# Kernel tuning notes

Hardware: AMD Instinct MI355X
Metric: run time of the kernel (lower is better)

## Reference

```python
import jax, jax.numpy as jnp
import numpy as np

EPS = 1e-5  # BatchNorm eps (torch default); BN is in training mode with gamma=1, beta=0 (init values)


def bn(x, axes):
    m = jnp.mean(x, axis=axes, keepdims=True)
    v = jnp.var(x, axis=axes, keepdims=True)
    return (x - m) * jax.lax.rsqrt(v + EPS)


def knn_idx(xyz, k):
    # brute-force squared-distance matrix [B,N,N], k smallest
    d = jnp.sum((xyz[:, :, None, :] - xyz[:, None, :, :]) ** 2, axis=-1)
    _, idx = jax.lax.top_k(-d, k)
    return idx  # [B,N,k]


def gather(x, idx):
    # x: [B,N,C], idx: [B,N,k] -> [B,N,k,C]
    return jax.vmap(lambda a, i: a[i])(x, idx)


def lse(xyz, features, idx, w):
    nbr_xyz = gather(xyz, idx)                       # [B,N,k,3]
    rel = nbr_xyz - xyz[:, :, None, :]
    dist = jnp.sqrt(jnp.maximum(jnp.sum(rel ** 2, -1, keepdims=True), 1e-12))
    nbr_f = gather(features, idx)                    # [B,N,k,C]
    enc = jnp.concatenate([rel, dist, nbr_f], -1)    # [B,N,k,C+4]
    return jax.nn.relu(bn(jnp.einsum('bnkc,oc->bnko', enc, w), (0, 1, 2)))


def att_pool(x, sw1, sw2, sb2, mw):
    # x: [B,N,k,C]
    h = jax.nn.relu(bn(jnp.einsum('bnkc,oc->bnko', x, sw1), (0, 1, 2)))
    scores = jax.nn.softmax(jnp.einsum('bnkc,oc->bnko', h, sw2) + sb2, axis=2)  # softmax over k
    feat = jnp.sum(x * scores, axis=2)               # [B,N,C]
    return jax.nn.relu(bn(jnp.einsum('bnc,oc->bno', feat, mw), (0, 1)))


def drb(x, w1, w2):
    # in_channels == out_channels -> identity shortcut
    h = jax.nn.relu(bn(jnp.einsum('bnc,oc->bno', x, w1), (0, 1)))
    h = bn(jnp.einsum('bnc,oc->bno', h, w2), (0, 1))
    return jax.nn.relu(h + x)


def setup_inputs() -> dict:
    key = jax.random.key(0)
    B, N, C, K, OUT = 4, 8192, 32, 16, 128
    H = OUT // 2  # 64
    ks = jax.random.split(key, 16)
    s = 0.05
    return {
        'xyz': jax.random.normal(ks[0], (B, N, 3), jnp.float32),
        'features': jax.random.normal(ks[1], (B, N, C), jnp.float32),
        'w_lse1': jax.random.normal(ks[2], (H, C + 4), jnp.float32) * s,
        'w_lse2': jax.random.normal(ks[3], (H, C + 4), jnp.float32) * s,
        'ap1_sw1': jax.random.normal(ks[4], (H, H), jnp.float32) * s,
        'ap1_sw2': jax.random.normal(ks[5], (1, H), jnp.float32) * s,
        'ap1_sb2': jax.random.normal(ks[6], (1,), jnp.float32) * s,
        'ap1_mw': jax.random.normal(ks[7], (H, H), jnp.float32) * s,
        'ap2_sw1': jax.random.normal(ks[8], (H, H), jnp.float32) * s,
        'ap2_sw2': jax.random.normal(ks[9], (1, H), jnp.float32) * s,
        'ap2_sb2': jax.random.normal(ks[10], (1,), jnp.float32) * s,
        'ap2_mw': jax.random.normal(ks[11], (H, H), jnp.float32) * s,
        'drb_w1': jax.random.normal(ks[12], (OUT, OUT), jnp.float32) * s,
        'drb_w2': jax.random.normal(ks[13], (OUT, OUT), jnp.float32) * s,
    }


def reference(xyz, features, w_lse1, w_lse2, ap1_sw1, ap1_sw2, ap1_sb2, ap1_mw,
              ap2_sw1, ap2_sw2, ap2_sb2, ap2_mw, drb_w1, drb_w2):
    K = 16
    idx = knn_idx(xyz, K)  # original calls knn twice on same xyz -> identical indices
    f1 = att_pool(lse(xyz, features, idx, w_lse1), ap1_sw1, ap1_sw2, ap1_sb2, ap1_mw)
    f2 = att_pool(lse(xyz, features, idx, w_lse2), ap2_sw1, ap2_sw2, ap2_sb2, ap2_mw)
    agg = jnp.concatenate([f1, f2], axis=-1)  # [B,N,128]
    return drb(agg, drb_w1, drb_w2)           # [B,N,128]
```

## Files before the change

### kernel.cpp

```cpp
#include <hip/hip_runtime.h>
#include <hip/hip_bf16.h>
#include <hip/hip_fp16.h>
#include <float.h>
#include <math.h>

#define DEVFN __device__ __forceinline__

DEVFN void wavefence() { __builtin_amdgcn_wave_barrier(); }

using half8 = __attribute__((ext_vector_type(8))) _Float16;
using f32x4 = __attribute__((ext_vector_type(4))) float;

namespace {
constexpr int Bq = 4, Nq = 8192, Cq = 32, Kq = 16;
constexpr int PTS = Bq * Nq;
constexpr int CH = 16;
constexpr int CAND = Nq / CH;
constexpr double ROWS = 524288.0;

constexpr int DS_Y = 0, DS_Z = 256, DS_G = 512, DS_H1 = 768, DS_H2 = 1024;

constexpr size_t OFF_KD   = 0;
constexpr size_t OFF_KJ   = (size_t)32 << 20;
constexpr size_t OFF_X0   = 0;
constexpr size_t OFF_X1   = (size_t)64 << 20;
constexpr size_t OFF_ENC  = (size_t)128 << 20;
constexpr size_t OFF_H1   = 0;
constexpr size_t OFF_H2   = (size_t)16 << 20;
constexpr size_t OFF_GRAW = (size_t)192 << 20;
constexpr size_t OFF_AGG  = (size_t)208 << 20;
constexpr size_t OFF_IDX  = (size_t)224 << 20;
constexpr size_t OFF_DST  = (size_t)226 << 20;
constexpr size_t OFF_MST  = ((size_t)226 << 20) + 10240;
constexpr size_t OFF_BNP  = ((size_t)226 << 20) + 16384;
constexpr size_t WS_NEED  = ((size_t)226 << 20) + 32768;
constexpr size_t FB_GRAW  = (size_t)64 << 20;
constexpr size_t FB_AGG   = (size_t)80 << 20;
constexpr size_t FB_H1    = (size_t)96 << 20;
constexpr size_t FB_H2    = (size_t)112 << 20;
constexpr size_t FB_IDX   = (size_t)128 << 20;
constexpr size_t FB_DST   = (size_t)130 << 20;
constexpr size_t FB_MST   = ((size_t)130 << 20) + 10240;
constexpr size_t FB_BNP   = ((size_t)130 << 20) + 16384;
}

DEVFN void ce_asc(float& a, float& b) {
  const float lo = fminf(a, b), hi = fmaxf(a, b);
  a = lo; b = hi;
}

DEVFN void topk16_update(float* __restrict__ L, float* __restrict__ d) {
#pragma unroll
  for (int k = 2; k <= 16; k <<= 1) {
#pragma unroll
    for (int j = k >> 1; j > 0; j >>= 1) {
#pragma unroll
      for (int i = 0; i < 16; ++i) {
        const int l = i ^ j;
        if (l > i) {
          if ((i & k) == 0) {
            const float lo = fminf(d[i], d[l]), hi = fmaxf(d[i], d[l]);
            d[i] = lo; d[l] = hi;
          } else {
            const float lo = fminf(d[i], d[l]), hi = fmaxf(d[i], d[l]);
            d[i] = hi; d[l] = lo;
          }
        }
      }
    }
  }
#pragma unroll
  for (int i = 0; i < 16; ++i) L[i] = fminf(L[i], d[15 - i]);
#pragma unroll
  for (int j = 8; j > 0; j >>= 1) {
#pragma unroll
    for (int i = 0; i < 16; ++i) {
      const int l = i ^ j;
      if (l > i) ce_asc(L[i], L[l]);
    }
  }
}

DEVFN float distf(const float4 c, const float qx, const float qy, const float qz) {
  const float dx = qx - c.x, dy = qy - c.y, dz = qz - c.z;
  return __fadd_rn(__fadd_rn(__fmul_rn(dx, dx), __fmul_rn(dy, dy)), __fmul_rn(dz, dz));
}

__global__ __launch_bounds__(256, 4) void knn_chunk_kernel(const float* __restrict__ xyz,
                                                           float* __restrict__ pd,
                                                           int* __restrict__ pj) {
  const int b = blockIdx.z;
  const int ch = blockIdx.y;
  const int n = blockIdx.x * 256 + threadIdx.x;
  __shared__ __align__(16) float4 tile[CAND];
  const float* xb = xyz + (size_t)b * Nq * 3;
  for (int t = threadIdx.x; t < CAND; t += 256) {
    const int j = ch * CAND + t;
    tile[t] = make_float4(xb[j * 3], xb[j * 3 + 1], xb[j * 3 + 2], 0.f);
  }
  __syncthreads();
  const float qx = xb[n * 3], qy = xb[n * 3 + 1], qz = xb[n * 3 + 2];
  float L[16];
#pragma unroll
  for (int i = 0; i < 16; ++i) L[i] = FLT_MAX;
  for (int t = 0; t < CAND; t += 16) {
    float d[16];
#pragma unroll
    for (int u = 0; u < 16; ++u) d[u] = distf(tile[t + u], qx, qy, qz);
    topk16_update(L, d);
  }
  const float kth = L[15];
  const size_t base = (((size_t)b * Nq + n) * CH + ch) * Kq;
  int cnt = 0, tfirst = -1;
  for (int t = 0; t < CAND; ++t) {
    const float d = distf(tile[t], qx, qy, qz);
    if (d < kth) { pd[base + cnt] = d; pj[base + cnt] = ch * CAND + t; ++cnt; }
    tfirst = (d == kth && tfirst < 0) ? t : tfirst;
  }
  if (cnt == 15) {
    pd[base + 15] = kth; pj[base + 15] = ch * CAND + tfirst; cnt = 16;
  }
  if (__any(cnt < 16)) {
    for (int t = 0; t < CAND; ++t) {
      const float d = distf(tile[t], qx, qy, qz);
      if (d == kth && cnt < 16) { pd[base + cnt] = d; pj[base + cnt] = ch * CAND + t; ++cnt; }
    }
  }
}

__global__ __launch_bounds__(256, 4) void knn_merge_kernel(const float* __restrict__ pd,
                                                           const int* __restrict__ pj,
                                                           int* __restrict__ idxo) {
  const int q = blockIdx.x * 256 + threadIdx.x;
  const float* dp = pd + (size_t)q * CH * Kq;
  const int* jp = pj + (size_t)q * CH * Kq;
  float L[16];
#pragma unroll
  for (int i = 0; i < 16; ++i) L[i] = FLT_MAX;
  for (int t = 0; t < CH * Kq; t += 16) {
    float d[16];
#pragma unroll
    for (int u = 0; u < 16; u += 4) {
      const float4 v = *(const float4*)(dp + t + u);
      d[u] = v.x; d[u + 1] = v.y; d[u + 2] = v.z; d[u + 3] = v.w;
    }
    topk16_update(L, d);
  }
  const float kth = L[15];
  int* op = idxo + (size_t)q * Kq;
  int cnt = 0;
  for (int t = 0; t < CH * Kq; ++t) {
    const float d = dp[t];
    if (d < kth) { op[cnt] = jp[t]; ++cnt; }
  }
  for (int t = 0; t < CH * Kq; ++t) {
    const float d = dp[t];
    if (d == kth && cnt < 16) { op[cnt] = jp[t]; ++cnt; }
  }
}

struct PF { float4 f0, f1; float nx, ny, nz; };

DEVFN PF issue_feat(const float* __restrict__ features, const float* __restrict__ xyz,
                    int p, int j, int sub) {
  const int b = p >> 13;
  const float* fr = features + ((size_t)b * Nq + j) * Cq;
  const float* xb = xyz + ((size_t)b * Nq + j) * 3;
  PF r;
  r.f0 = *(const float4*)(fr + sub * 8);
  r.f1 = *(const float4*)(fr + sub * 8 + 4);
  r.nx = xb[0]; r.ny = xb[1]; r.nz = xb[2];
  return r;
}

DEVFN int issue_idx(const int* __restrict__ idx, int p, int lane) {
  return idx[(size_t)p * Kq + (lane >> 2)];
}

DEVFN float3 issue_query(const float* __restrict__ xyz, int p) {
  const float* q = xyz + (size_t)p * 3;
  return make_float3(q[0], q[1], q[2]);
}

DEVFN void commit_enc(__half* __restrict__ enc, int lane, const PF& pf,
                      float qx, float qy, float qz) {
  const int k = lane >> 2, sub = lane & 3;
  __half* er = enc + k * 40;
  union { float4 f; __half2 h[4]; } u;
  u.h[0] = __floats2half2_rn(pf.f0.x, pf.f0.y);
  u.h[1] = __floats2half2_rn(pf.f0.z, pf.f0.w);
  u.h[2] = __floats2half2_rn(pf.f1.x, pf.f1.y);
  u.h[3] = __floats2half2_rn(pf.f1.z, pf.f1.w);
  *(float4*)(er + sub * 8) = u.f;
  if (sub == 0) {
    const float rx = pf.nx - qx, ry = pf.ny - qy, rz = pf.nz - qz;
    const float ss = rx * rx + ry * ry + rz * rz;
    const float dd = sqrtf(fmaxf(ss, 1e-12f));
    __half2* rd = (__half2*)(er + 32);
    rd[0] = __floats2half2_rn(rx, ry);
    rd[1] = __floats2half2_rn(rz, dd);
  }
}

DEVFN void zero_enc_pad(__half* __restrict__ enc, int lane) {
  if (lane < 16) {
    const __half2 z2 = __floats2half2_rn(0.f, 0.f);
    __half2* pz = (__half2*)(enc + lane * 40 + 36);
    pz[0] = z2; pz[1] = z2;
  }
}

DEVFN float dot40h(const __half* __restrict__ er, const __half2* __restrict__ wh2) {
  float a0 = 0.f, a1 = 0.f, a2 = 0.f, a3 = 0.f;
#pragma unroll
  for (int r = 0; r < 5; ++r) {
    union { float4 f; __half2 h[4]; } u;
    u.f = *(const float4*)(er + r * 8);
#pragma unroll
    for (int q = 0; q < 4; ++q) {
      const __half2 xv = u.h[q];
      const __half2 wv = wh2[r * 4 + q];
      if (q & 1) {
        a2 += __low2float(xv) * __low2float(wv);
        a3 += __high2float(xv) * __high2float(wv);
      } else {
        a0 += __low2float(xv) * __low2float(wv);
        a1 += __high2float(xv) * __high2float(wv);
      }
    }
  }
  return (a0 + a1) + (a2 + a3);
}

DEVFN float dot64x(const __half* __restrict__ xr, const __half2* __restrict__ sh2) {
  float a0 = 0.f, a1 = 0.f, a2 = 0.f, a3 = 0.f;
#pragma unroll
  for (int r = 0; r < 8; ++r) {
    union { float4 f; __half2 h[4]; } u;
    u.f = *(const float4*)(xr + r * 8);
#pragma unroll
    for (int q = 0; q < 4; ++q) {
      const __half2 xv = u.h[q];
      const __half2 wv = sh2[r * 4 + q];
      if (q & 1) {
        a2 += __low2float(xv) * __low2float(wv);
        a3 += __high2float(xv) * __high2float(wv);
      } else {
        a0 += __low2float(xv) * __low2float(wv);
        a1 += __high2float(xv) * __high2float(wv);
      }
    }
  }
  return (a0 + a1) + (a2 + a3);
}

DEVFN void load_w40(const float* __restrict__ Wrow, __half2* wh2) {
#pragma unroll
  for (int c = 0; c < 16; ++c)
    wh2[c] = __floats2half2_rn(Wrow[4 + 2 * c], Wrow[5 + 2 * c]);
  wh2[16] = __floats2half2_rn(Wrow[0], Wrow[1]);
  wh2[17] = __floats2half2_rn(Wrow[2], Wrow[3]);
  wh2[18] = __floats2half2_rn(0.f, 0.f);
  wh2[19] = wh2[18];
}

DEVFN void load_b1(const float* __restrict__ W, int lane, half8* b1) {
  const int o16 = lane & 15, q = lane >> 4;
#pragma unroll
  for (int t = 0; t < 4; ++t) {
    const int o = t * 16 + o16;
#pragma unroll
    for (int ks = 0; ks < 2; ++ks) {
      half8 v;
#pragma unroll
      for (int j = 0; j < 8; ++j) {
        const int s = ks * 32 + q * 8 + j;
        float wv = 0.f;
        if (s < 36) { const int orig = (s < 32) ? (s + 4) : (s - 32); wv = W[o * 36 + orig]; }
        v[j] = (_Float16)wv;
      }
      b1[t * 2 + ks] = v;
    }
  }
}

DEVFN void load_b2(const float* __restrict__ S1, int lane, half8* b2) {
  const int o16 = lane & 15, q = lane >> 4;
#pragma unroll
  for (int t = 0; t < 4; ++t) {
    const int o = t * 16 + o16;
#pragma unroll
    for (int ks = 0; ks < 2; ++ks) {
      half8 v;
#pragma unroll
      for (int j = 0; j < 8; ++j) {
        const int c = ks * 32 + q * 8 + j;
        v[j] = (_Float16)S1[o * 64 + c];
      }
      b2[t * 2 + ks] = v;
    }
  }
}

#define GATHER_PROLOGUE                                                      \
  int p = wid;                                                               \
  int jc = issue_idx(idx, p, lane);                                          \
  PF cur = issue_feat(features, xyz, p, jc, lane & 3);                       \
  float3 qc = issue_query(xyz, p);                                           \
  int pn0 = p + nw; if (pn0 >= PTS) pn0 = p;                                 \
  int jn = issue_idx(idx, pn0, lane);                                        \
  float3 qn = issue_query(xyz, pn0);                                         \
  for (; p < PTS; p += nw) {                                                 \
    int pn = p + nw; if (pn >= PTS) pn = p;                                  \
    int pn2 = pn + nw; if (pn2 >= PTS) pn2 = pn;                             \
    PF nxt = issue_feat(features, xyz, pn, jn, lane & 3);                    \
    const int jn2 = issue_idx(idx, pn2, lane);                               \
    const float3 q2 = issue_query(xyz, pn2);                                 \
    commit_enc(enc, lane, cur, qc.x, qc.y, qc.z);                            \
    wavefence();

#define GATHER_EPILOGUE                                                      \
    wavefence();                                                             \
    cur = nxt; qc = qn; qn = q2; jn = jn2;                                   \
  }

__global__ __launch_bounds__(256) void encM_kernel(const float* __restrict__ xyz,
                                                   const float* __restrict__ features,
                                                   const int* __restrict__ idx,
                                                   float* __restrict__ mstat,
                                                   __half* __restrict__ encb) {
  __shared__ __align__(16) __half encS[4][16 * 40];
  __shared__ float mred[4][36 * 37];
  const int lane = threadIdx.x & 63, wv = threadIdx.x >> 6;
  __half* enc = encS[wv];
  zero_enc_pad(enc, lane);
  wavefence();
  const int li = (lane < 36) ? lane : 0;
  float macc[36];
#pragma unroll
  for (int i = 0; i < 36; ++i) macc[i] = 0.f;
  float vacc = 0.f;
  const int wid = blockIdx.x * 4 + wv, nw = gridDim.x * 4;
  GATHER_PROLOGUE
#pragma unroll
    for (int k = 0; k < 16; ++k) {
      const __half* er = enc + k * 40;
      const float ei = __half2float(er[li]);
      vacc += ei;
#pragma unroll
      for (int r = 0; r < 5; ++r) {
        union { float4 f; __half2 h[4]; } u;
        u.f = *(const float4*)(er + r * 8);
#pragma unroll
        for (int q = 0; q < 4; ++q) {
          const int s = r * 8 + 2 * q;
          if (s < 36)     macc[s]     += ei * __low2float(u.h[q]);
          if (s + 1 < 36) macc[s + 1] += ei * __high2float(u.h[q]);
        }
      }
    }
    if (encb) {
#pragma unroll
      for (int it = 0; it < 2; ++it) {
        const int c = it * 64 + lane;
        if (c < 80) {
          const float4 v = *(const float4*)((const char*)enc + c * 16);
          *(float4*)((char*)encb + (size_t)p * 1280 + c * 16) = v;
        }
      }
    }
  GATHER_EPILOGUE
  if (lane < 36) {
#pragma unroll
    for (int j = 0; j < 36; ++j) mred[wv][lane * 37 + j] = macc[j];
    mred[wv][lane * 37 + 36] = vacc;
  }
  __syncthreads();
  for (int t = threadIdx.x; t < 36 * 37; t += 256) {
    const float s = mred[0][t] + mred[1][t] + mred[2][t] + mred[3][t];
    atomicAdd(&mstat[t], s);
  }
}

__global__ void y_finalize_kernel(const float* __restrict__ mstat,
                                  const float* __restrict__ wl1,
                                  const float* __restrict__ wl2,
                                  float* __restrict__ bnp) {
  const int t = threadIdx.x;
  const int br = t >> 6, o = t & 63;
  const float* W = br ? wl2 : wl1;
  double wrow[36];
  for (int s = 0; s < 36; ++s) {
    const int orig = (s < 32) ? (s + 4) : (s - 32);
    wrow[s] = (double)W[o * 36 + orig];
  }
  double mean = 0.0, ey2 = 0.0;
  for (int i = 0; i < 36; ++i) {
    mean += wrow[i] * (double)mstat[i * 37 + 36];
    double rowacc = 0.0;
    for (int j = 0; j < 36; ++j) rowacc += wrow[j] * (double)mstat[i * 37 + j];
    ey2 += wrow[i] * rowacc;
  }
  const double invR = 1.0 / ROWS;
  mean *= invR; ey2 *= invR;
  const double var = ey2 - mean * mean;
  bnp[DS_Y + br * 64 + o] = (float)mean;
  bnp[DS_Y + 128 + br * 64 + o] = (float)(1.0 / sqrt(var + 1e-5));
}

__global__ void bn_finalize_kernel(const double* __restrict__ dstat, float* __restrict__ bnp,
                                   int base, double invc) {
  const int t = threadIdx.x;
  const double m = dstat[base + t] * invc;
  const double v = dstat[base + 128 + t] * invc - m * m;
  bnp[base + t] = (float)m;
  bnp[base + 128 + t] = (float)(1.0 / sqrt(v + 1e-5));
}

__global__ __launch_bounds__(256)
void passA2s_kernel(const __half* __restrict__ encbuf,
                    const float* __restrict__ wl1,
                    const float* __restrict__ wl2,
                    const float* __restrict__ bnp,
                    __half* __restrict__ x0buf,
                    __half* __restrict__ x1buf) {
  __shared__ __align__(16) __half xS[4][16 * 64];
  const int lane = threadIdx.x & 63, wv = threadIdx.x >> 6;
  __half* xL = xS[wv];
  half8 b1a[8], b1b[8];
  load_b1(wl1, lane, b1a);
  load_b1(wl2, lane, b1b);
  const int r16 = lane & 15, q4 = lane >> 4;
  float ym0[4], ys0[4], ym1[4], ys1[4];
#pragma unroll
  for (int t = 0; t < 4; ++t) {
    ym0[t] = bnp[DS_Y + t * 16 + r16];
    ys0[t] = bnp[DS_Y + 128 + t * 16 + r16];
    ym1[t] = bnp[DS_Y + 64 + t * 16 + r16];
    ys1[t] = bnp[DS_Y + 128 + 64 + t * 16 + r16];
  }
  const int wid = blockIdx.x * 4 + wv, nw = gridDim.x * 4;
  for (int p = wid; p < PTS; p += nw) {
    const size_t eb = (size_t)p * 640 + r16 * 40 + q4 * 8;
    const half8 a0 = *(const half8*)(encbuf + eb);
    half8 a1;
#pragma unroll
    for (int j = 0; j < 8; ++j) a1[j] = (_Float16)0.f;
    if (q4 == 0) a1 = *(const half8*)(encbuf + eb + 32);
    {
      f32x4 yt[4];
#pragma unroll
      for (int t = 0; t < 4; ++t) {
        f32x4 acc = {0.f, 0.f, 0.f, 0.f};
        acc = __builtin_amdgcn_mfma_f32_16x16x32_f16(a0, b1a[t * 2], acc, 0, 0, 0);
        acc = __builtin_amdgcn_mfma_f32_16x16x32_f16(a1, b1a[t * 2 + 1], acc, 0, 0, 0);
        yt[t] = acc;
      }
#pragma unroll
      for (int t = 0; t < 4; ++t) {
        const int col = t * 16 + r16;
        const int chk = col >> 3;
#pragma unroll
        for (int rr = 0; rr < 4; ++rr) {
          const int row = q4 * 4 + rr;
          float xv = (yt[t][rr] - ym0[t]) * ys0[t];
          xv = xv > 0.f ? xv : 0.f;
          *(_Float16*)((char*)xL + row * 128 + ((chk ^ (row & 7)) * 16) + (col & 7) * 2) =
              (_Float16)xv;
        }
      }
      wavefence();
#pragma unroll
      for (int it = 0; it < 2; ++it) {
        const int chunk = it * 64 + lane;
        const int row = chunk >> 3, c8 = chunk & 7;
        const float4 xv4 = *(const float4*)((const char*)xL + row * 128 + ((c8 ^ (row & 7)) * 16));
        *(float4*)((char*)x0buf + (size_t)p * 2048 + chunk * 16) = xv4;
      }
      wavefence();
    }
    {
      f32x4 yt[4];
#pragma unroll
      for (int t = 0; t < 4; ++t) {
        f32x4 acc = {0.f, 0.f, 0.f, 0.f};
        acc = __builtin_amdgcn_mfma_f32_16x16x32_f16(a0, b1b[t * 2], acc, 0, 0, 0);
        acc = __builtin_amdgcn_mfma_f32_16x16x32_f16(a1, b1b[t * 2 + 1], acc, 0, 0, 0);
        yt[t] = acc;
      }
#pragma unroll
      for (int t = 0; t < 4; ++t) {
        const int col = t * 16 + r16;
        const int chk = col >> 3;
#pragma unroll
        for (int rr = 0; rr < 4; ++rr) {
          const int row = q4 * 4 + rr;
          float xv = (yt[t][rr] - ym1[t]) * ys1[t];
          xv = xv > 0.f ? xv : 0.f;
          *(_Float16*)((char*)xL + row * 128 + ((chk ^ (row & 7)) * 16) + (col & 7) * 2) =
              (_Float16)xv;
        }
      }
      wavefence();
#pragma unroll
      for (int it = 0; it < 2; ++it) {
        const int chunk = it * 64 + lane;
        const int row = chunk >> 3, c8 = chunk & 7;
        const float4 xv4 = *(const float4*)((const char*)xL + row * 128 + ((c8 ^ (row & 7)) * 16));
        *(float4*)((char*)x1buf + (size_t)p * 2048 + chunk * 16) = xv4;
      }
      wavefence();
    }
  }
}

__global__ __launch_bounds__(256)
void zstat_kernel(const __half* __restrict__ x0, const __half* __restrict__ x1,
                  const float* __restrict__ s1a, const float* __restrict__ s1b,
                  double* __restrict__ dstat) {
  const int lane = threadIdx.x & 63, wv = threadIdx.x >> 6;
  half8 b2a[8], b2b[8];
  load_b2(s1a, lane, b2a);
  load_b2(s1b, lane, b2b);
  const int r16 = lane & 15, q4 = lane >> 4;
  float sa1[4] = {0.f, 0.f, 0.f, 0.f}, sa2[4] = {0.f, 0.f, 0.f, 0.f};
  float sb1[4] = {0.f, 0.f, 0.f, 0.f}, sb2s[4] = {0.f, 0.f, 0.f, 0.f};
  const int wid = blockIdx.x * 4 + wv, nw = gridDim.x * 4;
  for (int p = wid; p < PTS; p += nw) {
    const size_t abase = (size_t)p * 1024 + r16 * 64 + q4 * 8;
    const half8 xa0 = *(const half8*)(x0 + abase);
    const half8 xa1 = *(const half8*)(x0 + abase + 32);
    const half8 xb0 = *(const half8*)(x1 + abase);
    const half8 xb1 = *(const half8*)(x1 + abase + 32);
#pragma unroll
    for (int t = 0; t < 4; ++t) {
      f32x4 acc = {0.f, 0.f, 0.f, 0.f};
      acc = __builtin_amdgcn_mfma_f32_16x16x32_f16(xa0, b2a[t * 2], acc, 0, 0, 0);
      acc = __builtin_amdgcn_mfma_f32_16x16x32_f16(xa1, b2a[t * 2 + 1], acc, 0, 0, 0);
#pragma unroll
      for (int rr = 0; rr < 4; ++rr) { const float zv = acc[rr]; sa1[t] += zv; sa2[t] += zv * zv; }
      f32x4 acc2 = {0.f, 0.f, 0.f, 0.f};
      acc2 = __builtin_amdgcn_mfma_f32_16x16x32_f16(xb0, b2b[t * 2], acc2, 0, 0, 0);
      acc2 = __builtin_amdgcn_mfma_f32_16x16x32_f16(xb1, b2b[t * 2 + 1], acc2, 0, 0, 0);
#pragma unroll
      for (int rr = 0; rr < 4; ++rr) { const float zv = acc2[rr]; sb1[t] += zv; sb2s[t] += zv * zv; }
    }
  }
#pragma unroll
  for (int t = 0; t < 4; ++t) {
    sa1[t] += __shfl_xor(sa1[t], 16, 64);  sa1[t] += __shfl_xor(sa1[t], 32, 64);
    sa2[t] += __shfl_xor(sa2[t], 16, 64);  sa2[t] += __shfl_xor(sa2[t], 32, 64);
    sb1[t] += __shfl_xor(sb1[t], 16, 64);  sb1[t] += __shfl_xor(sb1[t], 32, 64);
    sb2s[t] += __shfl_xor(sb2s[t], 16, 64); sb2s[t] += __shfl_xor(sb2s[t], 32, 64);
  }
  if (lane < 16) {
#pragma unroll
    for (int t = 0; t < 4; ++t) {
      atomicAdd(&dstat[DS_Z + t * 16 + lane], (double)sa1[t]);
      atomicAdd(&dstat[DS_Z + 128 + t * 16 + lane], (double)sa2[t]);
      atomicAdd(&dstat[DS_Z + 64 + t * 16 + lane], (double)sb1[t]);
      atomicAdd(&dstat[DS_Z + 128 + 64 + t * 16 + lane], (double)sb2s[t]);
    }
  }
}

__global__ __launch_bounds__(256)
void passB2_mat_kernel(const __half* __restrict__ xbuf,
                       const float* __restrict__ S1,
                       const float* __restrict__ s2,
                       const float* __restrict__ sb,
                       const float* __restrict__ mw,
                       const float* __restrict__ bnp,
                       double* __restrict__ dstat,
                       float* __restrict__ graw,
                       int br) {
  __shared__ __align__(16) __half2 mwl2[64 * 34];
  __shared__ __align__(16) float featL[4][64];
  __shared__ __align__(16) float zS[4][16 * 64];
  for (int t = threadIdx.x; t < 64 * 32; t += 256) {
    const int r = t >> 5, c2 = t & 31;
    mwl2[r * 34 + c2] = __floats2half2_rn(mw[r * 64 + c2 * 2], mw[r * 64 + c2 * 2 + 1]);
  }
  __syncthreads();
  const int lane = threadIdx.x & 63, wv = threadIdx.x >> 6;
  const int r16 = lane & 15, q4 = lane >> 4;
  half8 b2[8];
  load_b2(S1, lane, b2);
  const __half2* mrow = mwl2 + lane * 34;
  const float zm = bnp[DS_Z + br * 64 + lane];
  const float zsc = bnp[DS_Z + 128 + br * 64 + lane];
  const float sw2r = s2[lane];
  const float sb2v = sb[0];
  float gs1 = 0.f, gs2 = 0.f;
  float* zw = &zS[wv][0];
  const int wid = blockIdx.x * 4 + wv, nw = gridDim.x * 4;
  for (int p = wid; p < PTS; p += nw) {
    const size_t abase = (size_t)p * 1024 + r16 * 64 + q4 * 8;
    const half8 xa0 = *(const half8*)(xbuf + abase);
    const half8 xa1 = *(const half8*)(xbuf + abase + 32);
#pragma unroll
    for (int t = 0; t < 4; ++t) {
      f32x4 acc = {0.f, 0.f, 0.f, 0.f};
      acc = __builtin_amdgcn_mfma_f32_16x16x32_f16(xa0, b2[t * 2], acc, 0, 0, 0);
      acc = __builtin_amdgcn_mfma_f32_16x16x32_f16(xa1, b2[t * 2 + 1], acc, 0, 0, 0);
#pragma unroll
      for (int rr = 0; rr < 4; ++rr)
        zw[(q4 * 4 + rr) * 64 + t * 16 + r16] = acc[rr];
    }
    wavefence();
    const __half* xr = xbuf + (size_t)p * 1024 + lane;
    const float* zr = zw + lane;
    float xv[16], pl[16];
#pragma unroll
    for (int k = 0; k < 16; ++k) {
      xv[k] = __half2float(xr[k * 64]);
      float h = (zr[k * 64] - zm) * zsc;
      h = h > 0.f ? h : 0.f;
      pl[k] = h * sw2r;
    }
#pragma unroll
    for (int off = 1; off < 64; off <<= 1) {
#pragma unroll
      for (int k = 0; k < 16; ++k) pl[k] += __shfl_xor(pl[k], off, 64);
    }
    float mx = -FLT_MAX;
#pragma unroll
    for (int k = 0; k < 16; ++k) { pl[k] += sb2v; mx = fmaxf(mx, pl[k]); }
    float se = 0.f;
#pragma unroll
    for (int k = 0; k < 16; ++k) { pl[k] = expf(pl[k] - mx); se += pl[k]; }
    const float inv = 1.f / se;
    float f = 0.f;
#pragma unroll
    for (int k = 0; k < 16; ++k) f += xv[k] * (pl[k] * inv);
    featL[wv][lane] = f;
    wavefence();
    const float* featW = &featL[wv][0];
    float g0 = 0.f, g1 = 0.f, g2 = 0.f, g3 = 0.f;
#pragma unroll
    for (int c8 = 0; c8 < 8; ++c8) {
      const float4 fa = *(const float4*)(featW + c8 * 8);
      const float4 fb = *(const float4*)(featW + c8 * 8 + 4);
      const __half2 m0 = mrow[c8 * 4 + 0];
      const __half2 m1 = mrow[c8 * 4 + 1];
      const __half2 m2 = mrow[c8 * 4 + 2];
      const __half2 m3 = mrow[c8 * 4 + 3];
      g0 += fa.x * __low2float(m0); g1 += fa.y * __high2float(m0);
      g2 += fa.z * __low2float(m1); g3 += fa.w * __high2float(m1);
      g0 += fb.x * __low2float(m2); g1 += fb.y * __high2float(m2);
      g2 += fb.z * __low2float(m3); g3 += fb.w * __high2float(m3);
    }
    const float g = (g0 + g1) + (g2 + g3);
    graw[((size_t)br * PTS + p) * 64 + lane] = g;
    gs1 += g; gs2 += g * g;
    wavefence();
  }
  atomicAdd(&dstat[DS_G + br * 64 + lane], (double)gs1);
  atomicAdd(&dstat[DS_G + 128 + br * 64 + lane], (double)gs2);
}

__global__ __launch_bounds__(256)
void passA_kernel(const float* __restrict__ xyz,
                  const float* __restrict__ features,
                  const int* __restrict__ idx,
                  const float* __restrict__ wl1,
                  const float* __restrict__ wl2,
                  const float* __restrict__ s1a,
                  const float* __restrict__ s1b,
                  const float* __restrict__ bnp,
                  double* __restrict__ dstat) {
  const int br = blockIdx.y;
  const float* W = br ? wl2 : wl1;
  const float* S1 = br ? s1b : s1a;
  __shared__ __align__(16) __half encS[4][16 * 40];
  __shared__ __align__(16) __half xS[4][16 * 64];
  const int lane = threadIdx.x & 63, wv = threadIdx.x >> 6;
  __half* enc = encS[wv];
  __half* xL = xS[wv];
  zero_enc_pad(enc, lane);
  wavefence();
  __half2 wh2[20];
  load_w40(W + lane * 36, wh2);
  __half2 sh2[32];
#pragma unroll
  for (int c = 0; c < 32; ++c)
    sh2[c] = __floats2half2_rn(S1[lane * 64 + 2 * c], S1[lane * 64 + 2 * c + 1]);
  const float ym = bnp[DS_Y + br * 64 + lane];
  const float ys = bnp[DS_Y + 128 + br * 64 + lane];
  float zs1 = 0.f, zs2 = 0.f;
  const int wid = blockIdx.x * 4 + wv, nw = gridDim.x * 4;
  GATHER_PROLOGUE
#pragma unroll
    for (int k = 0; k < 16; ++k) {
      float xv = (dot40h(enc + k * 40, wh2) - ym) * ys;
      xv = xv > 0.f ? xv : 0.f;
      xL[k * 64 + lane] = __float2half(xv);
    }
    wavefence();
#pragma unroll
    for (int k = 0; k < 16; ++k) {
      const float acc = dot64x(xL + k * 64, sh2);
      zs1 += acc; zs2 += acc * acc;
    }
  GATHER_EPILOGUE
  atomicAdd(&dstat[DS_Z + br * 64 + lane], (double)zs1);
  atomicAdd(&dstat[DS_Z + 128 + br * 64 + lane], (double)zs2);
}

__global__ __launch_bounds__(256)
void passB_kernel(const float* __restrict__ xyz,
                  const float* __restrict__ features,
                  const int* __restrict__ idx,
                  const float* __restrict__ wl1,
                  const float* __restrict__ wl2,
                  const float* __restrict__ s1a,
                  const float* __restrict__ s1b,
                  const float* __restrict__ s2a,
                  const float* __restrict__ s2b,
                  const float* __restrict__ sba,
                  const float* __restrict__ sbb,
                  const float* __restrict__ mwa,
                  const float* __restrict__ mwb,
                  const float* __restrict__ bnp,
                  double* __restrict__ dstat,
                  float* __restrict__ graw) {
  const int br = blockIdx.y;
  const float* W = br ? wl2 : wl1;
  const float* S1 = br ? s1b : s1a;
  const float* S2 = br ? s2b : s2a;
  const float* SB = br ? sbb : sba;
  const float* MW = br ? mwb : mwa;
  __shared__ __align__(16) __half2 mwl2[64 * 34];
  __shared__ __align__(16) __half encS[4][16 * 40];
  __shared__ __align__(16) __half xS[4][16 * 64];
  __shared__ __align__(16) float featL[4][64];
  for (int t = threadIdx.x; t < 64 * 32; t += 256) {
    const int r = t >> 5, c2 = t & 31;
    mwl2[r * 34 + c2] = __floats2half2_rn(MW[r * 64 + c2 * 2], MW[r * 64 + c2 * 2 + 1]);
  }
  __syncthreads();
  const int lane = threadIdx.x & 63, wv = threadIdx.x >> 6;
  __half* enc = encS[wv];
  __half* xL = xS[wv];
  zero_enc_pad(enc, lane);
  wavefence();
  const __half2* mrow = mwl2 + lane * 34;
  __half2 wh2[20];
  load_w40(W + lane * 36, wh2);
  __half2 sh2[32];
#pragma unroll
  for (int c = 0; c < 32; ++c)
    sh2[c] = __floats2half2_rn(S1[lane * 64 + 2 * c], S1[lane * 64 + 2 * c + 1]);
  const float ym = bnp[DS_Y + br * 64 + lane];
  const float ys = bnp[DS_Y + 128 + br * 64 + lane];
  const float zm = bnp[DS_Z + br * 64 + lane];
  const float zs = bnp[DS_Z + 128 + br * 64 + lane];
  const float sw2r = S2[lane];
  const float sb2v = SB[0];
  float gs1 = 0.f, gs2 = 0.f;
  const int wid = blockIdx.x * 4 + wv, nw = gridDim.x * 4;
  GATHER_PROLOGUE
#pragma unroll
    for (int k = 0; k < 16; ++k) {
      float xv = (dot40h(enc + k * 40, wh2) - ym) * ys;
      xv = xv > 0.f ? xv : 0.f;
      xL[k * 64 + lane] = __float2half(xv);
    }
    wavefence();
    float pl[16];
#pragma unroll
    for (int k = 0; k < 16; ++k) {
      float h = (dot64x(xL + k * 64, sh2) - zm) * zs;
      h = h > 0.f ? h : 0.f;
      pl[k] = h * sw2r;
    }
#pragma unroll
    for (int off = 1; off < 64; off <<= 1) {
#pragma unroll
      for (int k = 0; k < 16; ++k) pl[k] += __shfl_xor(pl[k], off, 64);
    }
    float mx = -FLT_MAX;
#pragma unroll
    for (int k = 0; k < 16; ++k) { pl[k] += sb2v; mx = fmaxf(mx, pl[k]); }
    float se = 0.f;
#pragma unroll
    for (int k = 0; k < 16; ++k) { pl[k] = expf(pl[k] - mx); se += pl[k]; }
    const float inv = 1.f / se;
    float f = 0.f;
#pragma unroll
    for (int k = 0; k < 16; ++k) f += __half2float(xL[k * 64 + lane]) * (pl[k] * inv);
    featL[wv][lane] = f;
    wavefence();
    const float* featW = &featL[wv][0];
    float g0 = 0.f, g1 = 0.f, g2 = 0.f, g3 = 0.f;
#pragma unroll
    for (int c8 = 0; c8 < 8; ++c8) {
      const float4 fa = *(const float4*)(featW + c8 * 8);
      const float4 fb = *(const float4*)(featW + c8 * 8 + 4);
      const __half2 m0 = mrow[c8 * 4 + 0];
      const __half2 m1 = mrow[c8 * 4 + 1];
      const __half2 m2 = mrow[c8 * 4 + 2];
      const __half2 m3 = mrow[c8 * 4 + 3];
      g0 += fa.x * __low2float(m0); g1 += fa.y * __high2float(m0);
      g2 += fa.z * __low2float(m1); g3 += fa.w * __high2float(m1);
      g0 += fb.x * __low2float(m2); g1 += fb.y * __high2float(m2);
      g2 += fb.z * __low2float(m3); g3 += fb.w * __high2float(m3);
    }
    const float g = (g0 + g1) + (g2 + g3);
    graw[((size_t)br * PTS + p) * 64 + lane] = g;
    gs1 += g; gs2 += g * g;
  GATHER_EPILOGUE
  atomicAdd(&dstat[DS_G + br * 64 + lane], (double)gs1);
  atomicAdd(&dstat[DS_G + 128 + br * 64 + lane], (double)gs2);
}

__global__ __launch_bounds__(256) void drb_mm_kernel(const float* __restrict__ in,
                                                     const float* __restrict__ wmat,
                                                     const float* __restrict__ bnp,
                                                     double* __restrict__ dstat,
                                                     float* __restrict__ aggout,
                                                     float* __restrict__ rowout,
                                                     int bpIn, int dsOut, int mode) {
  __shared__ __align__(16) float wlds[128 * 129];
  __shared__ __align__(16) float rowS[4][128];
  for (int t = threadIdx.x; t < 128 * 128; t += 256) wlds[(t >> 7) * 129 + (t & 127)] = wmat[t];
  __syncthreads();
  const int lane = threadIdx.x & 63, wv = threadIdx.x >> 6;
  const float m0 = bnp[bpIn + lane], s0 = bnp[bpIn + 128 + lane];
  const float m1 = bnp[bpIn + 64 + lane], s1 = bnp[bpIn + 128 + 64 + lane];
  float a1s0 = 0.f, a1s1 = 0.f, a2s0 = 0.f, a2s1 = 0.f;
  const int wid = blockIdx.x * 4 + wv, nw = gridDim.x * 4;
  for (int p = wid; p < PTS; p += nw) {
    float v0, v1;
    if (mode == 0) {
      v0 = in[(size_t)p * 64 + lane];
      v1 = in[(size_t)PTS * 64 + (size_t)p * 64 + lane];
    } else {
      v0 = in[(size_t)p * 128 + lane];
      v1 = in[(size_t)p * 128 + 64 + lane];
    }
    v0 = (v0 - m0) * s0; v0 = v0 > 0.f ? v0 : 0.f;
    v1 = (v1 - m1) * s1; v1 = v1 > 0.f ? v1 : 0.f;
    rowS[wv][lane] = v0;
    rowS[wv][64 + lane] = v1;
    if (aggout) {
      aggout[(size_t)p * 128 + lane] = v0;
      aggout[(size_t)p * 128 + 64 + lane] = v1;
    }
    wavefence();
#pragma unroll
    for (int h = 0; h < 2; ++h) {
      const int o = h * 64 + lane;
      float b0 = 0.f, b1 = 0.f, b2 = 0.f, b3 = 0.f;
#pragma unroll
      for (int c4 = 0; c4 < 32; ++c4) {
        const float4 rv = *(const float4*)(&rowS[wv][c4 * 4]);
        b0 += rv.x * wlds[o * 129 + c4 * 4 + 0];
        b1 += rv.y * wlds[o * 129 + c4 * 4 + 1];
        b2 += rv.z * wlds[o * 129 + c4 * 4 + 2];
        b3 += rv.w * wlds[o * 129 + c4 * 4 + 3];
      }
      const float acc = (b0 + b1) + (b2 + b3);
      rowout[(size_t)p * 128 + o] = acc;
      if (h == 0) { a1s0 += acc; a2s0 += acc * acc; }
      else        { a1s1 += acc; a2s1 += acc * acc; }
    }
    wavefence();
  }
  atomicAdd(&dstat[dsOut + lane], (double)a1s0);
  atomicAdd(&dstat[dsOut + 64 + lane], (double)a1s1);
  atomicAdd(&dstat[dsOut + 128 + lane], (double)a2s0);
  atomicAdd(&dstat[dsOut + 128 + 64 + lane], (double)a2s1);
}

__global__ __launch_bounds__(256) void final_kernel(const float* __restrict__ h2,
                                                    const float* __restrict__ agg,
                                                    const float* __restrict__ bnp,
                                                    float* __restrict__ out) {
  const size_t e = (size_t)blockIdx.x * 256 + threadIdx.x;
  const int ch = (int)(e & 127);
  const float m = bnp[DS_H2 + ch], s = bnp[DS_H2 + 128 + ch];
  float v = (h2[e] - m) * s + agg[e];
  out[e] = v > 0.f ? v : 0.f;
}

extern "C" void kernel_launch(void* const* d_in, const int* in_sizes, int n_in,
                              void* d_out, int out_size, void* d_ws, size_t ws_size,
                              hipStream_t stream) {
  (void)in_sizes; (void)n_in; (void)out_size;
  const float* xyz      = (const float*)d_in[0];
  const float* features = (const float*)d_in[1];
  const float* w_lse1   = (const float*)d_in[2];
  const float* w_lse2   = (const float*)d_in[3];
  const float* ap1_sw1  = (const float*)d_in[4];
  const float* ap1_sw2  = (const float*)d_in[5];
  const float* ap1_sb2  = (const float*)d_in[6];
  const float* ap1_mw   = (const float*)d_in[7];
  const float* ap2_sw1  = (const float*)d_in[8];
  const float* ap2_sw2  = (const float*)d_in[9];
  const float* ap2_sb2  = (const float*)d_in[10];
  const float* ap2_mw   = (const float*)d_in[11];
  const float* drb_w1   = (const float*)d_in[12];
  const float* drb_w2   = (const float*)d_in[13];

  char* ws = (char*)d_ws;
  const bool mat = (ws_size >= WS_NEED);

  float*  knn_d = (float*)(ws + OFF_KD);
  int*    knn_j = (int*)(ws + OFF_KJ);
  int*    idx   = (int*)(ws + (mat ? OFF_IDX : FB_IDX));
  double* dstat = (double*)(ws + (mat ? OFF_DST : FB_DST));
  float*  mstat = (float*)(ws + (mat ? OFF_MST : FB_MST));
  float*  bnp   = (float*)(ws + (mat ? OFF_BNP : FB_BNP));
  float*  graw  = (float*)(ws + (mat ? OFF_GRAW : FB_GRAW));
  float*  agg   = (float*)(ws + (mat ? OFF_AGG : FB_AGG));
  float*  h1    = (float*)(ws + (mat ? OFF_H1 : FB_H1));
  float*  h2    = (float*)(ws + (mat ? OFF_H2 : FB_H2));
  float*  out   = (float*)d_out;

  (void)hipMemsetAsync(dstat, 0, 1280 * sizeof(double) + 36 * 37 * sizeof(float), stream);

  knn_chunk_kernel<<<dim3(Nq / 256, CH, Bq), 256, 0, stream>>>(xyz, knn_d, knn_j);
  knn_merge_kernel<<<dim3(PTS / 256), 256, 0, stream>>>(knn_d, knn_j, idx);

  __half* encb = mat ? (__half*)(ws + OFF_ENC) : nullptr;
  encM_kernel<<<dim3(1280), 256, 0, stream>>>(xyz, features, idx, mstat, encb);
  y_finalize_kernel<<<1, 128, 0, stream>>>(mstat, w_lse1, w_lse2, bnp);

  if (mat) {
    __half* x0 = (__half*)(ws + OFF_X0);
    __half* x1 = (__half*)(ws + OFF_X1);
    passA2s_kernel<<<dim3(1024), 256, 0, stream>>>(encb, w_lse1, w_lse2, bnp, x0, x1);
    zstat_kernel<<<dim3(1024), 256, 0, stream>>>(x0, x1, ap1_sw1, ap2_sw1, dstat);
    bn_finalize_kernel<<<1, 128, 0, stream>>>(dstat, bnp, DS_Z, 1.0 / ROWS);
    passB2_mat_kernel<<<dim3(1024), 256, 0, stream>>>(x0, ap1_sw1, ap1_sw2, ap1_sb2,
                                                      ap1_mw, bnp, dstat, graw, 0);
    passB2_mat_kernel<<<dim3(1024), 256, 0, stream>>>(x1, ap2_sw1, ap2_sw2, ap2_sb2,
                                                      ap2_mw, bnp, dstat, graw, 1);
  } else {
    passA_kernel<<<dim3(640, 2), 256, 0, stream>>>(xyz, features, idx, w_lse1, w_lse2,
                                                   ap1_sw1, ap2_sw1, bnp, dstat);
    bn_finalize_kernel<<<1, 128, 0, stream>>>(dstat, bnp, DS_Z, 1.0 / ROWS);
    passB_kernel<<<dim3(512, 2), 256, 0, stream>>>(xyz, features, idx, w_lse1, w_lse2,
                                                   ap1_sw1, ap2_sw1, ap1_sw2, ap2_sw2,
                                                   ap1_sb2, ap2_sb2, ap1_mw, ap2_mw,
                                                   bnp, dstat, graw);
  }
  bn_finalize_kernel<<<1, 128, 0, stream>>>(dstat, bnp, DS_G, 1.0 / PTS);

  drb_mm_kernel<<<dim3(512), 256, 0, stream>>>(graw, drb_w1, bnp, dstat, agg, h1,
                                               DS_G, DS_H1, 0);
  bn_finalize_kernel<<<1, 128, 0, stream>>>(dstat, bnp, DS_H1, 1.0 / PTS);

  drb_mm_kernel<<<dim3(512), 256, 0, stream>>>(h1, drb_w2, bnp, dstat, nullptr, h2,
                                               DS_H1, DS_H2, 1);
  bn_finalize_kernel<<<1, 128, 0, stream>>>(dstat, bnp, DS_H2, 1.0 / PTS);

  final_kernel<<<dim3(PTS * 128 / 256), 256, 0, stream>>>(h2, agg, bnp, out);
}
```

Baseline: 1.276 ms.

## Fuse z-statistics into passA2s and merge both passB2 branches into one launch

The z-statistics GEMM and sum-of-squares accumulation now run inside passA2s, reading the freshly written activations from LDS. This removes the separate zstat kernel and its full re-read of x0/x1 from global memory. The two per-branch passB2 launches become a single launch with a 2D grid, where blockIdx.y picks the branch. In exchange passA2s holds more registers (two extra sets of B fragments plus accumulators), which may lower occupancy.

```diff
diff --git a/kernel.cpp b/kernel.cpp
--- a/kernel.cpp
+++ b/kernel.cpp
@@ -421,15 +421,20 @@
 void passA2s_kernel(const __half* __restrict__ encbuf,
                     const float* __restrict__ wl1,
                     const float* __restrict__ wl2,
+                    const float* __restrict__ s1a,
+                    const float* __restrict__ s1b,
                     const float* __restrict__ bnp,
+                    double* __restrict__ dstat,
                     __half* __restrict__ x0buf,
                     __half* __restrict__ x1buf) {
   __shared__ __align__(16) __half xS[4][16 * 64];
   const int lane = threadIdx.x & 63, wv = threadIdx.x >> 6;
   __half* xL = xS[wv];
-  half8 b1a[8], b1b[8];
+  half8 b1a[8], b1b[8], b2a[8], b2b[8];
   load_b1(wl1, lane, b1a);
   load_b1(wl2, lane, b1b);
+  load_b2(s1a, lane, b2a);
+  load_b2(s1b, lane, b2b);
   const int r16 = lane & 15, q4 = lane >> 4;
   float ym0[4], ys0[4], ym1[4], ys1[4];
 #pragma unroll
@@ -439,6 +444,8 @@
     ym1[t] = bnp[DS_Y + 64 + t * 16 + r16];
     ys1[t] = bnp[DS_Y + 128 + 64 + t * 16 + r16];
   }
+  float sa1[4] = {0.f, 0.f, 0.f, 0.f}, sa2[4] = {0.f, 0.f, 0.f, 0.f};
+  float sb1[4] = {0.f, 0.f, 0.f, 0.f}, sb2s[4] = {0.f, 0.f, 0.f, 0.f};
   const int wid = blockIdx.x * 4 + wv, nw = gridDim.x * 4;
   for (int p = wid; p < PTS; p += nw) {
     const size_t eb = (size_t)p * 640 + r16 * 40 + q4 * 8;
@@ -477,6 +484,17 @@
         const float4 xv4 = *(const float4*)((const char*)xL + row * 128 + ((c8 ^ (row & 7)) * 16));
         *(float4*)((char*)x0buf + (size_t)p * 2048 + chunk * 16) = xv4;
       }
+      const char* xlb = (const char*)xL + r16 * 128;
+      const half8 xa0 = *(const half8*)(xlb + (((q4)     ^ (r16 & 7)) * 16));
+      const half8 xa1 = *(const half8*)(xlb + (((4 + q4) ^ (r16 & 7)) * 16));
+#pragma unroll
+      for (int t = 0; t < 4; ++t) {
+        f32x4 acc = {0.f, 0.f, 0.f, 0.f};
+        acc = __builtin_amdgcn_mfma_f32_16x16x32_f16(xa0, b2a[t * 2], acc, 0, 0, 0);
+        acc = __builtin_amdgcn_mfma_f32_16x16x32_f16(xa1, b2a[t * 2 + 1], acc, 0, 0, 0);
+#pragma unroll
+        for (int rr = 0; rr < 4; ++rr) { const float zv = acc[rr]; sa1[t] += zv; sa2[t] += zv * zv; }
+      }
       wavefence();
     }
     {
@@ -509,41 +527,18 @@
         const float4 xv4 = *(const float4*)((const char*)xL + row * 128 + ((c8 ^ (row & 7)) * 16));
         *(float4*)((char*)x1buf + (size_t)p * 2048 + chunk * 16) = xv4;
       }
+      const char* xlb = (const char*)xL + r16 * 128;
+      const half8 xb0 = *(const half8*)(xlb + (((q4)     ^ (r16 & 7)) * 16));
+      const half8 xb1 = *(const half8*)(xlb + (((4 + q4) ^ (r16 & 7)) * 16));
+#pragma unroll
+      for (int t = 0; t < 4; ++t) {
+        f32x4 acc = {0.f, 0.f, 0.f, 0.f};
+        acc = __builtin_amdgcn_mfma_f32_16x16x32_f16(xb0, b2b[t * 2], acc, 0, 0, 0);
+        acc = __builtin_amdgcn_mfma_f32_16x16x32_f16(xb1, b2b[t * 2 + 1], acc, 0, 0, 0);
+#pragma unroll
+        for (int rr = 0; rr < 4; ++rr) { const float zv = acc[rr]; sb1[t] += zv; sb2s[t] += zv * zv; }
+      }
       wavefence();
-    }
-  }
-}
-
-__global__ __launch_bounds__(256)
-void zstat_kernel(const __half* __restrict__ x0, const __half* __restrict__ x1,
-                  const float* __restrict__ s1a, const float* __restrict__ s1b,
-                  double* __restrict__ dstat) {
-  const int lane = threadIdx.x & 63, wv = threadIdx.x >> 6;
-  half8 b2a[8], b2b[8];
-  load_b2(s1a, lane, b2a);
-  load_b2(s1b, lane, b2b);
-  const int r16 = lane & 15, q4 = lane >> 4;
-  float sa1[4] = {0.f, 0.f, 0.f, 0.f}, sa2[4] = {0.f, 0.f, 0.f, 0.f};
-  float sb1[4] = {0.f, 0.f, 0.f, 0.f}, sb2s[4] = {0.f, 0.f, 0.f, 0.f};
-  const int wid = blockIdx.x * 4 + wv, nw = gridDim.x * 4;
-  for (int p = wid; p < PTS; p += nw) {
-    const size_t abase = (size_t)p * 1024 + r16 * 64 + q4 * 8;
-    const half8 xa0 = *(const half8*)(x0 + abase);
-    const half8 xa1 = *(const half8*)(x0 + abase + 32);
-    const half8 xb0 = *(const half8*)(x1 + abase);
-    const half8 xb1 = *(const half8*)(x1 + abase + 32);
-#pragma unroll
-    for (int t = 0; t < 4; ++t) {
-      f32x4 acc = {0.f, 0.f, 0.f, 0.f};
-      acc = __builtin_amdgcn_mfma_f32_16x16x32_f16(xa0, b2a[t * 2], acc, 0, 0, 0);
-      acc = __builtin_amdgcn_mfma_f32_16x16x32_f16(xa1, b2a[t * 2 + 1], acc, 0, 0, 0);
-#pragma unroll
-      for (int rr = 0; rr < 4; ++rr) { const float zv = acc[rr]; sa1[t] += zv; sa2[t] += zv * zv; }
-      f32x4 acc2 = {0.f, 0.f, 0.f, 0.f};
-      acc2 = __builtin_amdgcn_mfma_f32_16x16x32_f16(xb0, b2b[t * 2], acc2, 0, 0, 0);
-      acc2 = __builtin_amdgcn_mfma_f32_16x16x32_f16(xb1, b2b[t * 2 + 1], acc2, 0, 0, 0);
-#pragma unroll
-      for (int rr = 0; rr < 4; ++rr) { const float zv = acc2[rr]; sb1[t] += zv; sb2s[t] += zv * zv; }
     }
   }
 #pragma unroll
@@ -565,15 +560,25 @@
 }
 
 __global__ __launch_bounds__(256)
-void passB2_mat_kernel(const __half* __restrict__ xbuf,
-                       const float* __restrict__ S1,
-                       const float* __restrict__ s2,
-                       const float* __restrict__ sb,
-                       const float* __restrict__ mw,
+void passB2_mat_kernel(const __half* __restrict__ x0,
+                       const __half* __restrict__ x1,
+                       const float* __restrict__ s1a,
+                       const float* __restrict__ s1b,
+                       const float* __restrict__ s2a,
+                       const float* __restrict__ s2b,
+                       const float* __restrict__ sba,
+                       const float* __restrict__ sbb,
+                       const float* __restrict__ mwa,
+                       const float* __restrict__ mwb,
                        const float* __restrict__ bnp,
                        double* __restrict__ dstat,
-                       float* __restrict__ graw,
-                       int br) {
+                       float* __restrict__ graw) {
+  const int br = blockIdx.y;
+  const __half* xbuf = br ? x1 : x0;
+  const float* S1 = br ? s1b : s1a;
+  const float* s2 = br ? s2b : s2a;
+  const float* sb = br ? sbb : sba;
+  const float* mw = br ? mwb : mwa;
   __shared__ __align__(16) __half2 mwl2[64 * 34];
   __shared__ __align__(16) float featL[4][64];
   __shared__ __align__(16) float zS[4][16 * 64];
@@ -930,13 +935,12 @@
   if (mat) {
     __half* x0 = (__half*)(ws + OFF_X0);
     __half* x1 = (__half*)(ws + OFF_X1);
-    passA2s_kernel<<<dim3(1024), 256, 0, stream>>>(encb, w_lse1, w_lse2, bnp, x0, x1);
-    zstat_kernel<<<dim3(1024), 256, 0, stream>>>(x0, x1, ap1_sw1, ap2_sw1, dstat);
+    passA2s_kernel<<<dim3(1024), 256, 0, stream>>>(encb, w_lse1, w_lse2,
+                                                   ap1_sw1, ap2_sw1, bnp, dstat, x0, x1);
     bn_finalize_kernel<<<1, 128, 0, stream>>>(dstat, bnp, DS_Z, 1.0 / ROWS);
-    passB2_mat_kernel<<<dim3(1024), 256, 0, stream>>>(x0, ap1_sw1, ap1_sw2, ap1_sb2,
-                                                      ap1_mw, bnp, dstat, graw, 0);
-    passB2_mat_kernel<<<dim3(1024), 256, 0, stream>>>(x1, ap2_sw1, ap2_sw2, ap2_sb2,
-                                                      ap2_mw, bnp, dstat, graw, 1);
+    passB2_mat_kernel<<<dim3(1024, 2), 256, 0, stream>>>(x0, x1, ap1_sw1, ap2_sw1,
+                                                         ap1_sw2, ap2_sw2, ap1_sb2, ap2_sb2,
+                                                         ap1_mw, ap2_mw, bnp, dstat, graw);
   } else {
     passA_kernel<<<dim3(640, 2), 256, 0, stream>>>(xyz, features, idx, w_lse1, w_lse2,
                                                    ap1_sw1, ap2_sw1, bnp, dstat);
```

Result: faster. 1.183 ms, median of 2 (-7.3%).
